# Kernel optimization log

Measured on AMD Instinct MI355X. Metric: run time of the kernel, lower is better.

The kernel has to match this reference:

```python
import jax, jax.numpy as jnp
import numpy as np

# Shapes: [n_boxes, batch, ch, H, W] as produced by Uncropper in the original module.
N_BOXES, BATCH, CH_KQ, CH_V, H, W = 32, 4, 64, 64, 80, 80


def setup_inputs() -> dict:
    key = jax.random.key(0)
    k1, k2, k3 = jax.random.split(key, 3)
    q_big = jax.random.normal(k1, (N_BOXES, BATCH, CH_KQ, H, W), dtype=jnp.float32)
    k_big = jax.random.normal(k2, (N_BOXES, BATCH, CH_KQ, H, W), dtype=jnp.float32)
    v_big = jax.random.normal(k3, (N_BOXES, BATCH, CH_V, H, W), dtype=jnp.float32)
    return {"q_big": q_big, "k_big": k_big, "v_big": v_big}


def reference(q_big, k_big, v_big):
    # Original loop: for i in range(n_boxes):
    #   w = softmax(sum(q_big[i] * k_big, dim=-3, keepdim=True) / sqrt(ch_kq), dim=-5)
    #   delta_big[i] = sum(w * v_big, dim=-5)
    # Vectorized: attention over the box axis, independent per (batch, h, w) pixel.
    scale = 1.0 / np.sqrt(q_big.shape[2]).astype(np.float32)
    # scores[i, j, b, h, w] = <q_big[i, b, :, h, w], k_big[j, b, :, h, w]>
    scores = jnp.einsum('ibchw,jbchw->ijbhw', q_big, k_big) * scale
    w = jax.nn.softmax(scores, axis=1)  # softmax over source box j (dim=-5 in torch)
    delta_big = jnp.einsum('ijbhw,jbchw->ibchw', w, v_big)
    return delta_big
```

## Files before the change

### kernel.cpp

```cpp
#include <hip/hip_runtime.h>


#define NBOX    32
#define NBATCH  4
#define CH      64
#define HW      6400
#define PIX     16
#define NT      512
#define NTILES  (HW / PIX)
#define NUNITS  (NBATCH * NTILES)

typedef __fp16 f16;
typedef f16   f16x2  __attribute__((ext_vector_type(2)));
typedef f16   f16x8  __attribute__((ext_vector_type(8)));
typedef float f32x16 __attribute__((ext_vector_type(16)));

#define SYNC() do { __builtin_amdgcn_sched_barrier(0); __syncthreads(); \
                    __builtin_amdgcn_sched_barrier(0); } while (0)

__device__ __forceinline__ int swz(int L) {
    return L ^ ((((L >> 9) & 3) | (((L >> 13) & 1) << 2)) << 4);
}
__device__ __forceinline__ int swzO(int L) {
    return L ^ ((((L >> 10) & 7) ^ ((L >> 5) & 7)) << 4);
}

#define ZERO16 {0.f,0.f,0.f,0.f,0.f,0.f,0.f,0.f,0.f,0.f,0.f,0.f,0.f,0.f,0.f,0.f}

__global__ __launch_bounds__(NT, 2)
void box_attn_mfma(const float* __restrict__ q, const float* __restrict__ k,
                   const float* __restrict__ v, float* __restrict__ out) {
    __shared__ char sm[65536];
    char* const KF = sm;
    char* const QF = sm + 32768;
    char* const VF = sm;
    char* const OB = sm + 32768;

    const int t    = threadIdx.x;
    const int lane = t & 63;
    const int w    = t >> 6;
    const int h    = lane >> 5;
    const int bid  = blockIdx.x;
    const int unit = (bid & 7) * (NUNITS / 8) + (bid >> 3);
    const int b    = unit / NTILES;
    const int p0   = (unit % NTILES) * PIX;

    auto stage_kq = [&](const float* __restrict__ src, char* reg_, int chalf) {
#pragma unroll
        for (int rep = 0; rep < 2; ++rep) {
            int u = rep * NT + t;
            int pxq = u & 3, qq = (u >> 2) & 3, kcL = (u >> 4) & 1, box = (u >> 5) & 31;
            int cb = chalf + kcL * 16 + qq * 4;
            const float* g = src + ((size_t)((box * NBATCH + b) * CH + cb)) * HW + p0 + pxq * 4;
            float4 l0 = *(const float4*)(g);
            float4 l1 = *(const float4*)(g + HW);
            float4 l2 = *(const float4*)(g + 2 * HW);
            float4 l3 = *(const float4*)(g + 3 * HW);
            const float* f0 = &l0.x; const float* f1 = &l1.x;
            const float* f2 = &l2.x; const float* f3 = &l3.x;
            int Lb = kcL * 1024 + (box + 32 * (qq & 1)) * 16 + (qq >> 1) * 8;
#pragma unroll
            for (int pi = 0; pi < 4; ++pi) {
                union { f16x2 hh[2]; uint2 u2; } val;
                val.hh[0] = __builtin_amdgcn_cvt_pkrtz(f0[pi], f1[pi]);
                val.hh[1] = __builtin_amdgcn_cvt_pkrtz(f2[pi], f3[pi]);
                *(uint2*)(reg_ + swz((pxq * 4 + pi) * 2048 + Lb)) = val.u2;
            }
        }
    };

    auto stage_v = [&](int coff) {
        const size_t JS = (size_t)NBATCH * CH * HW;
#pragma unroll
        for (int rep = 0; rep < 2; ++rep) {
            int u = rep * NT + t;
            int pxq = u & 3, qq = (u >> 2) & 3, jc = (u >> 4) & 1, cL = (u >> 5) & 31;
            const float* g = v + ((size_t)(((jc * 16 + qq * 4) * NBATCH + b) * CH + coff + cL)) * HW
                               + p0 + pxq * 4;
            float4 l0 = *(const float4*)(g);
            float4 l1 = *(const float4*)(g + JS);
            float4 l2 = *(const float4*)(g + 2 * JS);
            float4 l3 = *(const float4*)(g + 3 * JS);
            const float* f0 = &l0.x; const float* f1 = &l1.x;
            const float* f2 = &l2.x; const float* f3 = &l3.x;
            int Lb = jc * 1024 + (cL + 32 * (qq & 1)) * 16 + (qq >> 1) * 8;
#pragma unroll
            for (int pi = 0; pi < 4; ++pi) {
                union { f16x2 hh[2]; uint2 u2; } val;
                val.hh[0] = __builtin_amdgcn_cvt_pkrtz(f0[pi], f1[pi]);
                val.hh[1] = __builtin_amdgcn_cvt_pkrtz(f2[pi], f3[pi]);
                *(uint2*)(VF + swz((pxq * 4 + pi) * 2048 + Lb)) = val.u2;
            }
        }
    };

    auto smax_pack = [&](const f32x16& s, f16x8& fr0, f16x8& fr1) {
        float p[16];
        float m = s[0];
#pragma unroll
        for (int r = 1; r < 16; ++r) m = fmaxf(m, s[r]);
        m = fmaxf(m, __shfl_xor(m, 32, 64));
        float sum = 0.f;
#pragma unroll
        for (int r = 0; r < 16; ++r) { p[r] = __expf((s[r] - m) * 0.125f); sum += p[r]; }
        sum += __shfl_xor(sum, 32, 64);
        float inv = 1.f / sum;
        union { f16x8 v8; f16x2 hh[4]; } u0, u1;
#pragma unroll
        for (int kk = 0; kk < 4; ++kk) {
            u0.hh[kk] = __builtin_amdgcn_cvt_pkrtz(p[2 * kk] * inv,     p[2 * kk + 1] * inv);
            u1.hh[kk] = __builtin_amdgcn_cvt_pkrtz(p[8 + 2 * kk] * inv, p[9 + 2 * kk] * inv);
        }
        fr0 = u0.v8; fr1 = u1.v8;
    };

    f32x16 sA = ZERO16, sB = ZERO16;

    stage_kq(k, KF, 0);
    stage_kq(q, QF, 0);
    SYNC();
#pragma unroll
    for (int kcL = 0; kcL < 2; ++kcL) {
        int LA = kcL * 1024 + lane * 16;
        f16x8 a0 = *(const f16x8*)(KF + swz(w * 2048 + LA));
        f16x8 b0 = *(const f16x8*)(QF + swz(w * 2048 + LA));
        sA = __builtin_amdgcn_mfma_f32_32x32x16_f16(a0, b0, sA, 0, 0, 0);
        f16x8 a1 = *(const f16x8*)(KF + swz((w + 8) * 2048 + LA));
        f16x8 b1 = *(const f16x8*)(QF + swz((w + 8) * 2048 + LA));
        sB = __builtin_amdgcn_mfma_f32_32x32x16_f16(a1, b1, sB, 0, 0, 0);
    }
    SYNC();
    stage_kq(k, KF, 32);
    stage_kq(q, QF, 32);
    SYNC();
#pragma unroll
    for (int kcL = 0; kcL < 2; ++kcL) {
        int LA = kcL * 1024 + lane * 16;
        f16x8 a0 = *(const f16x8*)(KF + swz(w * 2048 + LA));
        f16x8 b0 = *(const f16x8*)(QF + swz(w * 2048 + LA));
        sA = __builtin_amdgcn_mfma_f32_32x32x16_f16(a0, b0, sA, 0, 0, 0);
        f16x8 a1 = *(const f16x8*)(KF + swz((w + 8) * 2048 + LA));
        f16x8 b1 = *(const f16x8*)(QF + swz((w + 8) * 2048 + LA));
        sB = __builtin_amdgcn_mfma_f32_32x32x16_f16(a1, b1, sB, 0, 0, 0);
    }
    SYNC();

    stage_v(0);
    f16x8 pA0, pA1, pB0, pB1;
    smax_pack(sA, pA0, pA1);
    smax_pack(sB, pB0, pB1);
    SYNC();

#pragma unroll
    for (int ct = 0; ct < 2; ++ct) {
        f32x16 oA = ZERO16, oB = ZERO16;
        {
            int LA = lane * 16;
            f16x8 av0 = *(const f16x8*)(VF + swz(w * 2048 + LA));
            oA = __builtin_amdgcn_mfma_f32_32x32x16_f16(av0, pA0, oA, 0, 0, 0);
            f16x8 av1 = *(const f16x8*)(VF + swz((w + 8) * 2048 + LA));
            oB = __builtin_amdgcn_mfma_f32_32x32x16_f16(av1, pB0, oB, 0, 0, 0);
        }
        {
            int LA = 1024 + lane * 16;
            f16x8 av0 = *(const f16x8*)(VF + swz(w * 2048 + LA));
            oA = __builtin_amdgcn_mfma_f32_32x32x16_f16(av0, pA1, oA, 0, 0, 0);
            f16x8 av1 = *(const f16x8*)(VF + swz((w + 8) * 2048 + LA));
            oB = __builtin_amdgcn_mfma_f32_32x32x16_f16(av1, pB1, oB, 0, 0, 0);
        }
        const int i = lane & 31;
#pragma unroll
        for (int r = 0; r < 16; ++r) {
            int cL = (r & 3) + 8 * (r >> 2) + 4 * h;
            *(f16*)(OB + swzO(i * 1024 + cL * 32 + w * 2))       = (f16)oA[r];
            *(f16*)(OB + swzO(i * 1024 + cL * 32 + (w + 8) * 2)) = (f16)oB[r];
        }
        SYNC();

        if (ct == 0) stage_v(32);

#pragma unroll
        for (int rep = 0; rep < 2; ++rep) {
            int row = rep * NT + t;
            int oi = row >> 5, cL = row & 31;
            union { uint4 u4; f16x2 hh[4]; } ra, rb;
            ra.u4 = *(const uint4*)(OB + swzO(oi * 1024 + cL * 32));
            rb.u4 = *(const uint4*)(OB + swzO(oi * 1024 + cL * 32 + 16));
            float* op = out + ((size_t)((oi * NBATCH + b) * CH + ct * 32 + cL)) * HW + p0;
            float4 s0 = { (float)ra.hh[0][0], (float)ra.hh[0][1], (float)ra.hh[1][0], (float)ra.hh[1][1] };
            float4 s1 = { (float)ra.hh[2][0], (float)ra.hh[2][1], (float)ra.hh[3][0], (float)ra.hh[3][1] };
            float4 s2 = { (float)rb.hh[0][0], (float)rb.hh[0][1], (float)rb.hh[1][0], (float)rb.hh[1][1] };
            float4 s3 = { (float)rb.hh[2][0], (float)rb.hh[2][1], (float)rb.hh[3][0], (float)rb.hh[3][1] };
            *(float4*)(op + 0)  = s0;
            *(float4*)(op + 4)  = s1;
            *(float4*)(op + 8)  = s2;
            *(float4*)(op + 12) = s3;
        }
        if (ct == 0) SYNC();
    }
}

extern "C" void kernel_launch(void* const* d_in, const int* in_sizes, int n_in,
                              void* d_out, int out_size, void* d_ws, size_t ws_size,
                              hipStream_t stream) {
    const float* q = (const float*)d_in[0];
    const float* k = (const float*)d_in[1];
    const float* v = (const float*)d_in[2];
    float* o = (float*)d_out;
    dim3 grid(NUNITS);
    box_attn_mfma<<<grid, NT, 0, stream>>>(q, k, v, o);
}
```

Measured before the change: 232.0 us.

## Prefetch next K/Q/V chunks into registers before LDS staging phases

Splits each global-to-LDS staging step into a register load and a separate convert-and-store. The next channel half of K/Q, and then each V half, is loaded from global memory into registers while the current LDS contents are consumed by MFMA or softmax, so memory latency overlaps compute. This costs many extra VGPRs (24 float4 arrays, up to 16 float4 live at once) under launch_bounds(512,2), which risks spilling or lower occupancy.

```diff
diff --git a/kernel.cpp b/kernel.cpp
--- a/kernel.cpp
+++ b/kernel.cpp
@@ -45,31 +45,39 @@
     const int b    = unit / NTILES;
     const int p0   = (unit % NTILES) * PIX;
 
-    auto stage_kq = [&](const float* __restrict__ src, char* reg_, int chalf) {
+    auto load_kq = [&](const float* __restrict__ src, int chalf, float4* r) {
 #pragma unroll
         for (int rep = 0; rep < 2; ++rep) {
             int u = rep * NT + t;
             int pxq = u & 3, qq = (u >> 2) & 3, kcL = (u >> 4) & 1, box = (u >> 5) & 31;
             int cb = chalf + kcL * 16 + qq * 4;
             const float* g = src + ((size_t)((box * NBATCH + b) * CH + cb)) * HW + p0 + pxq * 4;
-            float4 l0 = *(const float4*)(g);
-            float4 l1 = *(const float4*)(g + HW);
-            float4 l2 = *(const float4*)(g + 2 * HW);
-            float4 l3 = *(const float4*)(g + 3 * HW);
-            const float* f0 = &l0.x; const float* f1 = &l1.x;
-            const float* f2 = &l2.x; const float* f3 = &l3.x;
+            r[rep * 4 + 0] = *(const float4*)(g);
+            r[rep * 4 + 1] = *(const float4*)(g + HW);
+            r[rep * 4 + 2] = *(const float4*)(g + 2 * HW);
+            r[rep * 4 + 3] = *(const float4*)(g + 3 * HW);
+        }
+    };
+    auto write_kq = [&](char* dst, const float4* r) {
+#pragma unroll
+        for (int rep = 0; rep < 2; ++rep) {
+            int u = rep * NT + t;
+            int pxq = u & 3, qq = (u >> 2) & 3, kcL = (u >> 4) & 1, box = (u >> 5) & 31;
             int Lb = kcL * 1024 + (box + 32 * (qq & 1)) * 16 + (qq >> 1) * 8;
+            const float* f0 = &r[rep * 4 + 0].x;
+            const float* f1 = &r[rep * 4 + 1].x;
+            const float* f2 = &r[rep * 4 + 2].x;
+            const float* f3 = &r[rep * 4 + 3].x;
 #pragma unroll
             for (int pi = 0; pi < 4; ++pi) {
                 union { f16x2 hh[2]; uint2 u2; } val;
                 val.hh[0] = __builtin_amdgcn_cvt_pkrtz(f0[pi], f1[pi]);
                 val.hh[1] = __builtin_amdgcn_cvt_pkrtz(f2[pi], f3[pi]);
-                *(uint2*)(reg_ + swz((pxq * 4 + pi) * 2048 + Lb)) = val.u2;
+                *(uint2*)(dst + swz((pxq * 4 + pi) * 2048 + Lb)) = val.u2;
             }
         }
     };
-
-    auto stage_v = [&](int coff) {
+    auto load_v = [&](int coff, float4* r) {
         const size_t JS = (size_t)NBATCH * CH * HW;
 #pragma unroll
         for (int rep = 0; rep < 2; ++rep) {
@@ -77,13 +85,22 @@
             int pxq = u & 3, qq = (u >> 2) & 3, jc = (u >> 4) & 1, cL = (u >> 5) & 31;
             const float* g = v + ((size_t)(((jc * 16 + qq * 4) * NBATCH + b) * CH + coff + cL)) * HW
                                + p0 + pxq * 4;
-            float4 l0 = *(const float4*)(g);
-            float4 l1 = *(const float4*)(g + JS);
-            float4 l2 = *(const float4*)(g + 2 * JS);
-            float4 l3 = *(const float4*)(g + 3 * JS);
-            const float* f0 = &l0.x; const float* f1 = &l1.x;
-            const float* f2 = &l2.x; const float* f3 = &l3.x;
+            r[rep * 4 + 0] = *(const float4*)(g);
+            r[rep * 4 + 1] = *(const float4*)(g + JS);
+            r[rep * 4 + 2] = *(const float4*)(g + 2 * JS);
+            r[rep * 4 + 3] = *(const float4*)(g + 3 * JS);
+        }
+    };
+    auto write_v = [&](const float4* r) {
+#pragma unroll
+        for (int rep = 0; rep < 2; ++rep) {
+            int u = rep * NT + t;
+            int pxq = u & 3, qq = (u >> 2) & 3, jc = (u >> 4) & 1, cL = (u >> 5) & 31;
             int Lb = jc * 1024 + (cL + 32 * (qq & 1)) * 16 + (qq >> 1) * 8;
+            const float* f0 = &r[rep * 4 + 0].x;
+            const float* f1 = &r[rep * 4 + 1].x;
+            const float* f2 = &r[rep * 4 + 2].x;
+            const float* f3 = &r[rep * 4 + 3].x;
 #pragma unroll
             for (int pi = 0; pi < 4; ++pi) {
                 union { f16x2 hh[2]; uint2 u2; } val;
@@ -115,9 +132,11 @@
     };
 
     f32x16 sA = ZERO16, sB = ZERO16;
-
-    stage_kq(k, KF, 0);
-    stage_kq(q, QF, 0);
+    float4 kr[8], qr[8], vr[8];
+
+    load_kq(k, 0, kr);  load_kq(q, 0, qr);
+    write_kq(KF, kr);   write_kq(QF, qr);
+    load_kq(k, 32, kr); load_kq(q, 32, qr);
     SYNC();
 #pragma unroll
     for (int kcL = 0; kcL < 2; ++kcL) {
@@ -130,8 +149,8 @@
         sB = __builtin_amdgcn_mfma_f32_32x32x16_f16(a1, b1, sB, 0, 0, 0);
     }
     SYNC();
-    stage_kq(k, KF, 32);
-    stage_kq(q, QF, 32);
+    write_kq(KF, kr); write_kq(QF, qr);
+    load_v(0, vr);
     SYNC();
 #pragma unroll
     for (int kcL = 0; kcL < 2; ++kcL) {
@@ -145,14 +164,14 @@
     }
     SYNC();
 
-    stage_v(0);
+    write_v(vr);
+    load_v(32, vr);
     f16x8 pA0, pA1, pB0, pB1;
     smax_pack(sA, pA0, pA1);
     smax_pack(sB, pB0, pB1);
     SYNC();
 
-#pragma unroll
-    for (int ct = 0; ct < 2; ++ct) {
+    {
         f32x16 oA = ZERO16, oB = ZERO16;
         {
             int LA = lane * 16;
@@ -177,7 +196,7 @@
         }
         SYNC();
 
-        if (ct == 0) stage_v(32);
+        write_v(vr);
 
 #pragma unroll
         for (int rep = 0; rep < 2; ++rep) {
@@ -186,7 +205,7 @@
             union { uint4 u4; f16x2 hh[4]; } ra, rb;
             ra.u4 = *(const uint4*)(OB + swzO(oi * 1024 + cL * 32));
             rb.u4 = *(const uint4*)(OB + swzO(oi * 1024 + cL * 32 + 16));
-            float* op = out + ((size_t)((oi * NBATCH + b) * CH + ct * 32 + cL)) * HW + p0;
+            float* op = out + ((size_t)((oi * NBATCH + b) * CH + cL)) * HW + p0;
             float4 s0 = { (float)ra.hh[0][0], (float)ra.hh[0][1], (float)ra.hh[1][0], (float)ra.hh[1][1] };
             float4 s1 = { (float)ra.hh[2][0], (float)ra.hh[2][1], (float)ra.hh[3][0], (float)ra.hh[3][1] };
             float4 s2 = { (float)rb.hh[0][0], (float)rb.hh[0][1], (float)rb.hh[1][0], (float)rb.hh[1][1] };
@@ -196,7 +215,50 @@
             *(float4*)(op + 8)  = s2;
             *(float4*)(op + 12) = s3;
         }
-        if (ct == 0) SYNC();
+        SYNC();
+    }
+    {
+        f32x16 oA = ZERO16, oB = ZERO16;
+        {
+            int LA = lane * 16;
+            f16x8 av0 = *(const f16x8*)(VF + swz(w * 2048 + LA));
+            oA = __builtin_amdgcn_mfma_f32_32x32x16_f16(av0, pA0, oA, 0, 0, 0);
+            f16x8 av1 = *(const f16x8*)(VF + swz((w + 8) * 2048 + LA));
+            oB = __builtin_amdgcn_mfma_f32_32x32x16_f16(av1, pB0, oB, 0, 0, 0);
+        }
+        {
+            int LA = 1024 + lane * 16;
+            f16x8 av0 = *(const f16x8*)(VF + swz(w * 2048 + LA));
+            oA = __builtin_amdgcn_mfma_f32_32x32x16_f16(av0, pA1, oA, 0, 0, 0);
+            f16x8 av1 = *(const f16x8*)(VF + swz((w + 8) * 2048 + LA));
+            oB = __builtin_amdgcn_mfma_f32_32x32x16_f16(av1, pB1, oB, 0, 0, 0);
+        }
+        const int i = lane & 31;
+#pragma unroll
+        for (int r = 0; r < 16; ++r) {
+            int cL = (r & 3) + 8 * (r >> 2) + 4 * h;
+            *(f16*)(OB + swzO(i * 1024 + cL * 32 + w * 2))       = (f16)oA[r];
+            *(f16*)(OB + swzO(i * 1024 + cL * 32 + (w + 8) * 2)) = (f16)oB[r];
+        }
+        SYNC();
+
+#pragma unroll
+        for (int rep = 0; rep < 2; ++rep) {
+            int row = rep * NT + t;
+            int oi = row >> 5, cL = row & 31;
+            union { uint4 u4; f16x2 hh[4]; } ra, rb;
+            ra.u4 = *(const uint4*)(OB + swzO(oi * 1024 + cL * 32));
+            rb.u4 = *(const uint4*)(OB + swzO(oi * 1024 + cL * 32 + 16));
+            float* op = out + ((size_t)((oi * NBATCH + b) * CH + 32 + cL)) * HW + p0;
+            float4 s0 = { (float)ra.hh[0][0], (float)ra.hh[0][1], (float)ra.hh[1][0], (float)ra.hh[1][1] };
+            float4 s1 = { (float)ra.hh[2][0], (float)ra.hh[2][1], (float)ra.hh[3][0], (float)ra.hh[3][1] };
+            float4 s2 = { (float)rb.hh[0][0], (float)rb.hh[0][1], (float)rb.hh[1][0], (float)rb.hh[1][1] };
+            float4 s3 = { (float)rb.hh[2][0], (float)rb.hh[2][1], (float)rb.hh[3][0], (float)rb.hh[3][1] };
+            *(float4*)(op + 0)  = s0;
+            *(float4*)(op + 4)  = s1;
+            *(float4*)(op + 8)  = s2;
+            *(float4*)(op + 12) = s3;
+        }
     }
 }
 
```

Result: faster. 221.6 us (-4.5%).
